# Kernel tuning notes

Measured on AMD Instinct MI355X. Metric: run time of the kernel, lower is better.

Reference implementation:

```python
import jax, jax.numpy as jnp
import numpy as np

N = 50000
E = 800000
C_IN = 256
HEADS = 4
HEAD_DIM = 32  # out_channels per head; concat=False -> final dim = HEAD_DIM


def setup_inputs() -> dict:
    key = jax.random.key(0)
    ks = jax.random.split(key, 10)
    s_in = 1.0 / np.sqrt(C_IN)
    return {
        "x": jax.random.normal(ks[0], (N, C_IN), dtype=jnp.float32),
        "edge_index": jax.random.randint(ks[1], (2, E), 0, N, dtype=jnp.int64),
        "Wq": jax.random.normal(ks[2], (C_IN, HEADS * HEAD_DIM), dtype=jnp.float32) * s_in,
        "bq": jax.random.normal(ks[3], (HEADS * HEAD_DIM,), dtype=jnp.float32) * 0.02,
        "Wk": jax.random.normal(ks[4], (C_IN, HEADS * HEAD_DIM), dtype=jnp.float32) * s_in,
        "bk": jax.random.normal(ks[5], (HEADS * HEAD_DIM,), dtype=jnp.float32) * 0.02,
        "Wv": jax.random.normal(ks[6], (C_IN, HEADS * HEAD_DIM), dtype=jnp.float32) * s_in,
        "bv": jax.random.normal(ks[7], (HEADS * HEAD_DIM,), dtype=jnp.float32) * 0.02,
        "Ws": jax.random.normal(ks[8], (C_IN, HEAD_DIM), dtype=jnp.float32) * s_in,
        "bs": jax.random.normal(ks[9], (HEAD_DIM,), dtype=jnp.float32) * 0.02,
    }


def reference(x, edge_index, Wq, bq, Wk, bk, Wv, bv, Ws, bs):
    n = x.shape[0]
    # Node-level projections, reshaped to (N, H, C)
    q = (x @ Wq + bq).reshape(n, HEADS, HEAD_DIM)
    k = (x @ Wk + bk).reshape(n, HEADS, HEAD_DIM)
    v = (x @ Wv + bv).reshape(n, HEADS, HEAD_DIM)

    src, dst = edge_index[0], edge_index[1]
    # Per-edge attention logits: (E, H)
    scale = 1.0 / jnp.sqrt(jnp.asarray(HEAD_DIM, dtype=x.dtype))
    logits = jnp.einsum("ehc,ehc->eh", q[dst], k[src]) * scale

    # Segment softmax over incoming edges of each destination node
    m = jax.ops.segment_max(logits, dst, num_segments=n)  # (N, H)
    e = jnp.exp(logits - m[dst])
    s = jax.ops.segment_sum(e, dst, num_segments=n)  # (N, H)
    alpha = e / s[dst]  # (E, H)

    # Weighted scatter-sum of values: (N, H, C)
    out = jax.ops.segment_sum(v[src] * alpha[..., None], dst, num_segments=n)
    # concat=False -> mean over heads; root skip connection
    out = out.mean(axis=1) + x @ Ws + bs  # (N, C)
    # LeakyReLU(0.1)
    return jnp.where(out > 0, out, 0.1 * out)
```

## Files before the change

### kernel.cpp

```cpp
#include <hip/hip_runtime.h>
#include <hip/hip_bf16.h>

#define NN 50000
#define EE 800000
#define CIN 256
#define HEADS 4
#define HDIM 32
#define GBM 64
#define CAP 64

#define OFF_C32 61440
#define OFF_BIAS 70656
#define LDS_BYTES 72320

typedef float f32x4 __attribute__((ext_vector_type(4)));
typedef __bf16 bf16x8 __attribute__((ext_vector_type(8)));

typedef const __attribute__((address_space(1))) unsigned int* gptr_t;
typedef __attribute__((address_space(3))) unsigned int* lptr_t;

static __device__ __forceinline__ unsigned short f2b(float f) {
    __hip_bfloat16 h = __float2bfloat16(f);
    return *(unsigned short*)&h;
}
static __device__ __forceinline__ float blo(unsigned int u) {
    union { unsigned int i; float f; } c; c.i = u << 16; return c.f;
}
static __device__ __forceinline__ float bhi(unsigned int u) {
    union { unsigned int i; float f; } c; c.i = u & 0xffff0000u; return c.f;
}

__global__ __launch_bounds__(256) void prep_w(
    const float* __restrict__ Wq, const float* __restrict__ Wk,
    const float* __restrict__ Wv, const float* __restrict__ Ws,
    const float* __restrict__ bq, const float* __restrict__ bk,
    const float* __restrict__ bv, const float* __restrict__ bs,
    unsigned short* __restrict__ WT, float* __restrict__ bias_cat) {
    const int t = blockIdx.x * 256 + threadIdx.x;
    if (t >= 416 * 256) return;
    const int c = t >> 8;
    const int k = t & 255;
    float w;
    if (c < 128)      w = Wq[k * 128 + c];
    else if (c < 256) w = Wk[k * 128 + (c - 128)];
    else if (c < 384) w = Wv[k * 128 + (c - 256)];
    else              w = Ws[k * 32 + (c - 384)];
    WT[t] = f2b(w);
    if (k == 0) {
        float b;
        if (c < 128)      b = bq[c];
        else if (c < 256) b = bk[c - 128];
        else if (c < 384) b = bv[c - 256];
        else              b = bs[c - 384];
        bias_cat[c] = b;
    }
}

__global__ __launch_bounds__(256, 2) void mfma_gemm(
    const float* __restrict__ x, const unsigned short* __restrict__ WT,
    const float* __restrict__ bias_cat,
    unsigned short* __restrict__ qb, unsigned short* __restrict__ kb,
    unsigned short* __restrict__ vb, float* __restrict__ skip) {
    __shared__ __align__(16) char U[LDS_BYTES];

    const int row0 = blockIdx.x * GBM;
    const int tid = threadIdx.x;
    const int wave = tid >> 6;
    const int lane = tid & 63;
    const int lr = lane & 15;
    const int lq = lane >> 4;

    float* biasL = (float*)(U + OFF_BIAS);
    for (int i = tid; i < 416; i += 256) biasL[i] = bias_cat[i];

    int grow_a = row0 + wave * 16 + lr;
    if (grow_a >= NN) grow_a = NN - 1;
    const float* xr = x + (size_t)grow_a * CIN;
    bf16x8 af[8];
    #pragma unroll
    for (int ks = 0; ks < 8; ++ks) {
        const float4 f0 = *(const float4*)(xr + ks * 32 + lq * 8);
        const float4 f1 = *(const float4*)(xr + ks * 32 + lq * 8 + 4);
        union { unsigned short us[8]; bf16x8 v; } o;
        o.us[0] = f2b(f0.x); o.us[1] = f2b(f0.y); o.us[2] = f2b(f0.z); o.us[3] = f2b(f0.w);
        o.us[4] = f2b(f1.x); o.us[5] = f2b(f1.y); o.us[6] = f2b(f1.z); o.us[7] = f2b(f1.w);
        af[ks] = o.v;
    }

    auto stageB = [&](int ct, int buf) {
        const int col0 = ct * 32;
        #pragma unroll
        for (int i = 0; i < 4; ++i) {
            const int u = i * 256 + tid;
            const int cB = u >> 5;
            const int ccs = (u & 31) ^ (cB & 7);
            __builtin_amdgcn_global_load_lds(
                (gptr_t)(const void*)(WT + (size_t)(col0 + cB) * CIN + ccs * 8),
                (lptr_t)(void*)(U + buf * 16384 + (i * 256 + (tid & 0xC0)) * 16),
                16, 0, 0);
        }
    };

    stageB(0, 0);
    __syncthreads();

    f32x4 acc[13][2] = {};
    #pragma unroll
    for (int ct = 0; ct < 13; ++ct) {
        if (ct < 12) stageB(ct + 1, (ct & 1) ^ 1);
        const unsigned short* Bc = (const unsigned short*)(U + (ct & 1) * 16384);
        #pragma unroll
        for (int ks = 0; ks < 8; ++ks) {
            const int cc = ks * 4 + lq;
            const bf16x8 b0 = *(const bf16x8*)(Bc + ((lr)      * 32 + (cc ^ (lr & 7))) * 8);
            const bf16x8 b1 = *(const bf16x8*)(Bc + ((16 + lr) * 32 + (cc ^ (lr & 7))) * 8);
            acc[ct][0] = __builtin_amdgcn_mfma_f32_16x16x32_bf16(af[ks], b0, acc[ct][0], 0, 0, 0);
            acc[ct][1] = __builtin_amdgcn_mfma_f32_16x16x32_bf16(af[ks], b1, acc[ct][1], 0, 0, 0);
        }
        __syncthreads();
    }

    unsigned short* C16 = (unsigned short*)U;
    float* C32 = (float*)(U + OFF_C32);
    const int rbase = wave * 16 + lq * 4;
    const int odd = lane & 1;
    #pragma unroll
    for (int ct = 0; ct < 12; ++ct) {
        #pragma unroll
        for (int j = 0; j < 2; ++j) {
            const float bme = biasL[ct * 32 + j * 16 + lr];
            unsigned int pr[4];
            #pragma unroll
            for (int r = 0; r < 4; ++r) {
                const float v = acc[ct][j][r] + bme;
                const float vn = __shfl_xor(v, 1);
                pr[r] = odd ? ((unsigned)f2b(vn) | ((unsigned)f2b(v) << 16))
                            : ((unsigned)f2b(v)  | ((unsigned)f2b(vn) << 16));
            }
            const unsigned int w0 = odd ? pr[2] : pr[0];
            const unsigned int w1 = odd ? pr[3] : pr[1];
            const int colp = j * 16 + (lr & ~1);
            const int rw = rbase + odd * 2;
            *(unsigned int*)(C16 + ct * 2560 + (rw    ) * 40 + colp) = w0;
            *(unsigned int*)(C16 + ct * 2560 + (rw + 1) * 40 + colp) = w1;
        }
    }
    #pragma unroll
    for (int j = 0; j < 2; ++j) {
        const float bme = biasL[384 + j * 16 + lr];
        #pragma unroll
        for (int r = 0; r < 4; ++r)
            C32[(rbase + r) * 36 + j * 16 + lr] = acc[12][j][r] + bme;
    }
    __syncthreads();

    const int srow = tid >> 2;
    const int schunk = tid & 3;
    const int gr2 = row0 + srow;
    if (gr2 < NN) {
        #pragma unroll
        for (int ct = 0; ct < 12; ++ct) {
            const uint4 val = *(const uint4*)(C16 + ct * 2560 + srow * 40 + schunk * 8);
            unsigned short* dst = (ct < 4) ? qb : (ct < 8) ? kb : vb;
            *(uint4*)(dst + (size_t)gr2 * 128 + (ct & 3) * 32 + schunk * 8) = val;
        }
        #pragma unroll
        for (int h = 0; h < 2; ++h) {
            const int ch = schunk + h * 4;
            const uint4 v = *(const uint4*)((const char*)C32 + srow * 144 + ch * 16);
            *(uint4*)(skip + (size_t)gr2 * 32 + ch * 4) = v;
        }
    }
}

__global__ __launch_bounds__(256) void fill_slots(const int* __restrict__ ei,
                                                  int* __restrict__ cnt,
                                                  unsigned short* __restrict__ slot) {
    const int t = blockIdx.x * 256 + threadIdx.x;
    if (t >= EE) return;
    const int dst = ei[EE + t];
    const int pos = atomicAdd(&cnt[dst], 1);
    if (pos < CAP) slot[(size_t)dst * CAP + pos] = (unsigned short)ei[t];
}

__global__ __launch_bounds__(256) void fused_edge(
    const unsigned short* __restrict__ qb, const unsigned short* __restrict__ kb,
    const unsigned short* __restrict__ vb, const unsigned short* __restrict__ slot,
    const int* __restrict__ cnt, const float* __restrict__ skip,
    float* __restrict__ out) {
    const int wid = blockIdx.x * 4 + (threadIdx.x >> 6);
    if (wid >= NN) return;
    const int lane = threadIdx.x & 63;
    const int sub = lane & 15;
    const int e4 = lane >> 4;

    const uint4 qu = *(const uint4*)(qb + (size_t)wid * 128 + sub * 8);
    float qf[8];
    qf[0] = blo(qu.x); qf[1] = bhi(qu.x); qf[2] = blo(qu.y); qf[3] = bhi(qu.y);
    qf[4] = blo(qu.z); qf[5] = bhi(qu.z); qf[6] = blo(qu.w); qf[7] = bhi(qu.w);

    const int deg = min(cnt[wid], CAP);
    const unsigned short* sl = slot + (size_t)wid * CAP;

    float s = 0.f;
    float acc[8] = {0.f, 0.f, 0.f, 0.f, 0.f, 0.f, 0.f, 0.f};

    for (int p0 = 0; p0 < deg; p0 += 4) {
        const int pe = p0 + e4;
        const bool valid = pe < deg;
        const int src = sl[valid ? pe : 0];
        const uint4 ku = *(const uint4*)(kb + (size_t)src * 128 + sub * 8);
        const uint4 vu = *(const uint4*)(vb + (size_t)src * 128 + sub * 8);

        float d = qf[0] * blo(ku.x) + qf[1] * bhi(ku.x)
                + qf[2] * blo(ku.y) + qf[3] * bhi(ku.y)
                + qf[4] * blo(ku.z) + qf[5] * bhi(ku.z)
                + qf[6] * blo(ku.w) + qf[7] * bhi(ku.w);
        d += __shfl_xor(d, 1);
        d += __shfl_xor(d, 2);
        const float w = valid ? __expf(d * 0.17677669529663687f) : 0.f;
        s += w;
        acc[0] += w * blo(vu.x); acc[1] += w * bhi(vu.x);
        acc[2] += w * blo(vu.y); acc[3] += w * bhi(vu.y);
        acc[4] += w * blo(vu.z); acc[5] += w * bhi(vu.z);
        acc[6] += w * blo(vu.w); acc[7] += w * bhi(vu.w);
    }

    s += __shfl_xor(s, 16); s += __shfl_xor(s, 32);
    #pragma unroll
    for (int j = 0; j < 8; ++j) {
        acc[j] += __shfl_xor(acc[j], 16);
        acc[j] += __shfl_xor(acc[j], 32);
    }
    const float inv = (s > 0.f) ? 0.25f / s : 0.f;
    #pragma unroll
    for (int j = 0; j < 8; ++j) acc[j] *= inv;
    #pragma unroll
    for (int j = 0; j < 8; ++j) {
        acc[j] += __shfl_xor(acc[j], 4);
        acc[j] += __shfl_xor(acc[j], 8);
    }

    if (lane < 4) {
        const float4 sk0 = *(const float4*)(skip + (size_t)wid * 32 + lane * 8);
        const float4 sk1 = *(const float4*)(skip + (size_t)wid * 32 + lane * 8 + 4);
        float o[8];
        o[0] = acc[0] + sk0.x; o[1] = acc[1] + sk0.y;
        o[2] = acc[2] + sk0.z; o[3] = acc[3] + sk0.w;
        o[4] = acc[4] + sk1.x; o[5] = acc[5] + sk1.y;
        o[6] = acc[6] + sk1.z; o[7] = acc[7] + sk1.w;
        #pragma unroll
        for (int j = 0; j < 8; ++j) o[j] = o[j] > 0.f ? o[j] : 0.1f * o[j];
        *(float4*)(out + (size_t)wid * 32 + lane * 8)     = make_float4(o[0], o[1], o[2], o[3]);
        *(float4*)(out + (size_t)wid * 32 + lane * 8 + 4) = make_float4(o[4], o[5], o[6], o[7]);
    }
}

extern "C" void kernel_launch(void* const* d_in, const int* in_sizes, int n_in,
                              void* d_out, int out_size, void* d_ws, size_t ws_size,
                              hipStream_t stream) {
    const float* x  = (const float*)d_in[0];
    const int*   ei = (const int*)d_in[1];
    const float* Wq = (const float*)d_in[2];
    const float* bq = (const float*)d_in[3];
    const float* Wk = (const float*)d_in[4];
    const float* bk = (const float*)d_in[5];
    const float* Wv = (const float*)d_in[6];
    const float* bv = (const float*)d_in[7];
    const float* Ws = (const float*)d_in[8];
    const float* bs = (const float*)d_in[9];
    float* out = (float*)d_out;

    char* ws = (char*)d_ws;
    size_t off = 0;
    auto alloc = [&](size_t bytes) { void* p = ws + off; off = (off + bytes + 255) & ~(size_t)255; return p; };
    unsigned short* WT   = (unsigned short*)alloc((size_t)416 * CIN * 2);
    float*          bc   = (float*)alloc((size_t)416 * 4);
    unsigned short* qb   = (unsigned short*)alloc((size_t)NN * 128 * 2);
    unsigned short* kb   = (unsigned short*)alloc((size_t)NN * 128 * 2);
    unsigned short* vb   = (unsigned short*)alloc((size_t)NN * 128 * 2);
    float*          skip = (float*)alloc((size_t)NN * HDIM * 4);
    int*            cnt  = (int*)alloc((size_t)NN * 4);
    unsigned short* slot = (unsigned short*)alloc((size_t)NN * CAP * 2);

    hipMemsetAsync(cnt, 0, (size_t)NN * 4, stream);

    prep_w<<<(416 * 256 + 255) / 256, 256, 0, stream>>>(Wq, Wk, Wv, Ws, bq, bk, bv, bs, WT, bc);

    fill_slots<<<(EE + 255) / 256, 256, 0, stream>>>(ei, cnt, slot);

    mfma_gemm<<<(NN + GBM - 1) / GBM, 256, 0, stream>>>(x, WT, bc, qb, kb, vb, skip);

    fused_edge<<<(NN + 3) / 4, 256, 0, stream>>>(qb, kb, vb, slot, cnt, skip, out);
}
```

Before: 241.3 us.

## Merge slot-fill into GEMM launch, fold memset into prep, shrink LDS epilogue

Clears the count array inside the weight-prep kernel, replacing the separate memset. Edge slot filling moves into the GEMM launch as extra blocks, so atomic scatter runs alongside the MFMA blocks. The GEMM epilogue now stages outputs through LDS in three passes instead of one, which roughly halves LDS use and may allow more resident blocks. This cuts two launches and overlaps memory-bound atomics with compute, at the cost of extra barriers in the epilogue and fill blocks that hold an LDS allocation they never use.

Measured after the change: 236.2 us. 2.1% less time.

```diff
diff --git a/kernel.cpp b/kernel.cpp
--- a/kernel.cpp
+++ b/kernel.cpp
@@ -8,10 +8,11 @@
 #define HDIM 32
 #define GBM 64
 #define CAP 64
-
-#define OFF_C32 61440
-#define OFF_BIAS 70656
-#define LDS_BYTES 72320
+#define NGB 782
+#define NFB 3125
+
+#define OFF_BIAS 32768
+#define LDS_BYTES 34432
 
 typedef float f32x4 __attribute__((ext_vector_type(4)));
 typedef __bf16 bf16x8 __attribute__((ext_vector_type(8)));
@@ -35,8 +36,10 @@
     const float* __restrict__ Wv, const float* __restrict__ Ws,
     const float* __restrict__ bq, const float* __restrict__ bk,
     const float* __restrict__ bv, const float* __restrict__ bs,
-    unsigned short* __restrict__ WT, float* __restrict__ bias_cat) {
+    unsigned short* __restrict__ WT, float* __restrict__ bias_cat,
+    int* __restrict__ cnt) {
     const int t = blockIdx.x * 256 + threadIdx.x;
+    if (t < NN) cnt[t] = 0;
     if (t >= 416 * 256) return;
     const int c = t >> 8;
     const int k = t & 255;
@@ -56,12 +59,23 @@
     }
 }
 
-__global__ __launch_bounds__(256, 2) void mfma_gemm(
+__global__ __launch_bounds__(256, 2) void gemm_and_fill(
     const float* __restrict__ x, const unsigned short* __restrict__ WT,
-    const float* __restrict__ bias_cat,
+    const float* __restrict__ bias_cat, const int* __restrict__ ei,
+    int* __restrict__ cnt, unsigned short* __restrict__ slot,
     unsigned short* __restrict__ qb, unsigned short* __restrict__ kb,
     unsigned short* __restrict__ vb, float* __restrict__ skip) {
     __shared__ __align__(16) char U[LDS_BYTES];
+
+    if (blockIdx.x >= NGB) {
+        const int t = (blockIdx.x - NGB) * 256 + threadIdx.x;
+        if (t < EE) {
+            const int dst = ei[EE + t];
+            const int pos = atomicAdd(&cnt[dst], 1);
+            if (pos < CAP) slot[(size_t)dst * CAP + pos] = (unsigned short)ei[t];
+        }
+        return;
+    }
 
     const int row0 = blockIdx.x * GBM;
     const int tid = threadIdx.x;
@@ -121,66 +135,66 @@
     }
 
     unsigned short* C16 = (unsigned short*)U;
-    float* C32 = (float*)(U + OFF_C32);
     const int rbase = wave * 16 + lq * 4;
     const int odd = lane & 1;
-    #pragma unroll
-    for (int ct = 0; ct < 12; ++ct) {
-        #pragma unroll
-        for (int j = 0; j < 2; ++j) {
-            const float bme = biasL[ct * 32 + j * 16 + lr];
-            unsigned int pr[4];
-            #pragma unroll
-            for (int r = 0; r < 4; ++r) {
-                const float v = acc[ct][j][r] + bme;
-                const float vn = __shfl_xor(v, 1);
-                pr[r] = odd ? ((unsigned)f2b(vn) | ((unsigned)f2b(v) << 16))
-                            : ((unsigned)f2b(v)  | ((unsigned)f2b(vn) << 16));
-            }
-            const unsigned int w0 = odd ? pr[2] : pr[0];
-            const unsigned int w1 = odd ? pr[3] : pr[1];
-            const int colp = j * 16 + (lr & ~1);
-            const int rw = rbase + odd * 2;
-            *(unsigned int*)(C16 + ct * 2560 + (rw    ) * 40 + colp) = w0;
-            *(unsigned int*)(C16 + ct * 2560 + (rw + 1) * 40 + colp) = w1;
-        }
-    }
-    #pragma unroll
-    for (int j = 0; j < 2; ++j) {
-        const float bme = biasL[384 + j * 16 + lr];
-        #pragma unroll
-        for (int r = 0; r < 4; ++r)
-            C32[(rbase + r) * 36 + j * 16 + lr] = acc[12][j][r] + bme;
-    }
-    __syncthreads();
-
     const int srow = tid >> 2;
     const int schunk = tid & 3;
     const int gr2 = row0 + srow;
-    if (gr2 < NN) {
+
+    #pragma unroll
+    for (int pass = 0; pass < 3; ++pass) {
         #pragma unroll
-        for (int ct = 0; ct < 12; ++ct) {
-            const uint4 val = *(const uint4*)(C16 + ct * 2560 + srow * 40 + schunk * 8);
-            unsigned short* dst = (ct < 4) ? qb : (ct < 8) ? kb : vb;
-            *(uint4*)(dst + (size_t)gr2 * 128 + (ct & 3) * 32 + schunk * 8) = val;
-        }
-        #pragma unroll
-        for (int h = 0; h < 2; ++h) {
-            const int ch = schunk + h * 4;
-            const uint4 v = *(const uint4*)((const char*)C32 + srow * 144 + ch * 16);
-            *(uint4*)(skip + (size_t)gr2 * 32 + ch * 4) = v;
-        }
-    }
-}
-
-__global__ __launch_bounds__(256) void fill_slots(const int* __restrict__ ei,
-                                                  int* __restrict__ cnt,
-                                                  unsigned short* __restrict__ slot) {
-    const int t = blockIdx.x * 256 + threadIdx.x;
-    if (t >= EE) return;
-    const int dst = ei[EE + t];
-    const int pos = atomicAdd(&cnt[dst], 1);
-    if (pos < CAP) slot[(size_t)dst * CAP + pos] = (unsigned short)ei[t];
+        for (int tt = 0; tt < 4; ++tt) {
+            const int ct = pass * 4 + tt;
+            #pragma unroll
+            for (int j = 0; j < 2; ++j) {
+                const float bme = biasL[ct * 32 + j * 16 + lr];
+                unsigned int pr[4];
+                #pragma unroll
+                for (int r = 0; r < 4; ++r) {
+                    const float v = acc[ct][j][r] + bme;
+                    const float vn = __shfl_xor(v, 1);
+                    pr[r] = odd ? ((unsigned)f2b(vn) | ((unsigned)f2b(v) << 16))
+                                : ((unsigned)f2b(v)  | ((unsigned)f2b(vn) << 16));
+                }
+                const unsigned int w0 = odd ? pr[2] : pr[0];
+                const unsigned int w1 = odd ? pr[3] : pr[1];
+                const int colp = j * 16 + (lr & ~1);
+                const int rw = rbase + odd * 2;
+                *(unsigned int*)(C16 + tt * 2560 + (rw    ) * 40 + colp) = w0;
+                *(unsigned int*)(C16 + tt * 2560 + (rw + 1) * 40 + colp) = w1;
+            }
+        }
+        if (pass == 2) {
+            float* C32 = (float*)(U + 20480);
+            #pragma unroll
+            for (int j = 0; j < 2; ++j) {
+                const float bme = biasL[384 + j * 16 + lr];
+                #pragma unroll
+                for (int r = 0; r < 4; ++r)
+                    C32[(rbase + r) * 36 + j * 16 + lr] = acc[12][j][r] + bme;
+            }
+        }
+        __syncthreads();
+        if (gr2 < NN) {
+            unsigned short* dstp = (pass == 0) ? qb : (pass == 1) ? kb : vb;
+            #pragma unroll
+            for (int tt = 0; tt < 4; ++tt) {
+                const uint4 val = *(const uint4*)(C16 + tt * 2560 + srow * 40 + schunk * 8);
+                *(uint4*)(dstp + (size_t)gr2 * 128 + tt * 32 + schunk * 8) = val;
+            }
+            if (pass == 2) {
+                const float* C32 = (const float*)(U + 20480);
+                #pragma unroll
+                for (int h = 0; h < 2; ++h) {
+                    const int ch = schunk + h * 4;
+                    const uint4 v = *(const uint4*)((const char*)C32 + srow * 144 + ch * 16);
+                    *(uint4*)(skip + (size_t)gr2 * 32 + ch * 4) = v;
+                }
+            }
+        }
+        if (pass < 2) __syncthreads();
+    }
 }
 
 __global__ __launch_bounds__(256) void fused_edge(
@@ -283,13 +297,9 @@
     int*            cnt  = (int*)alloc((size_t)NN * 4);
     unsigned short* slot = (unsigned short*)alloc((size_t)NN * CAP * 2);
 
-    hipMemsetAsync(cnt, 0, (size_t)NN * 4, stream);
-
-    prep_w<<<(416 * 256 + 255) / 256, 256, 0, stream>>>(Wq, Wk, Wv, Ws, bq, bk, bv, bs, WT, bc);
-
-    fill_slots<<<(EE + 255) / 256, 256, 0, stream>>>(ei, cnt, slot);
-
-    mfma_gemm<<<(NN + GBM - 1) / GBM, 256, 0, stream>>>(x, WT, bc, qb, kb, vb, skip);
+    prep_w<<<416, 256, 0, stream>>>(Wq, Wk, Wv, Ws, bq, bk, bv, bs, WT, bc, cnt);
+
+    gemm_and_fill<<<NGB + NFB, 256, 0, stream>>>(x, WT, bc, ei, cnt, slot, qb, kb, vb, skip);
 
     fused_edge<<<(NN + 3) / 4, 256, 0, stream>>>(qb, kb, vb, slot, cnt, skip, out);
 }
```
